# Optimization experiments

Hardware: AMD Instinct MI355X
Metric: run time of the kernel (lower is better)

The kernel has to match this reference:

```python
import jax, jax.numpy as jnp
import numpy as np

B, T, H = 4096, 64, 64        # sequences, time_step, n_hidden
OBS, ACT = 128, 32
EPS = 1e-12                    # tf.contrib layer_norm epsilon


def layer_norm(x, g, b):
    m = x.mean(-1, keepdims=True)
    v = x.var(-1, keepdims=True)
    return (x - m) * jax.lax.rsqrt(v + EPS) * g + b


def lstm_scan(xs, W, b):
    # xs: [T, B, D_in]; BasicLSTMCell with forget_bias=1.0
    h0 = jnp.zeros((xs.shape[1], H), xs.dtype)
    c0 = h0
    def step(carry, x_t):
        h, c = carry
        z = jnp.concatenate([x_t, h], axis=-1) @ W + b   # [B, 4H]
        i, j, f, o = jnp.split(z, 4, axis=-1)
        c = c * jax.nn.sigmoid(f + 1.0) + jax.nn.sigmoid(i) * jnp.tanh(j)
        h = jnp.tanh(c) * jax.nn.sigmoid(o)
        return (h, c), h
    _, hs = jax.lax.scan(step, (h0, c0), xs)
    return hs  # [T, B, H]


def setup_inputs() -> dict:
    key = jax.random.key(0)
    ks = jax.random.split(key, 10)
    u = lambda k, shp, s: jax.random.uniform(k, shp, jnp.float32, -s, s)
    return dict(
        obs=jax.random.normal(ks[0], (B * T, OBS), jnp.float32),
        action=jax.random.normal(ks[1], (B * T, ACT), jnp.float32),
        W1=u(ks[2], (OBS, 64), 0.1), b1=jnp.zeros(64), g1=jnp.ones(64), be1=jnp.zeros(64),
        W2=u(ks[3], (64 + ACT, 64), 0.1), b2=jnp.zeros(64), g2=jnp.ones(64), be2=jnp.zeros(64),
        Wf=u(ks[4], (64 + H, 4 * H), 0.08), bf=jnp.zeros(4 * H),
        Wb=u(ks[5], (64 + H, 4 * H), 0.08), bb=jnp.zeros(4 * H),
        wx=u(ks[6], (H,), 0.003), bx=jnp.zeros(()),
        wp=u(ks[7], (H,), 0.003), bp=jnp.zeros(()),
        gp=jnp.ones(T), bep=jnp.zeros(T),
        W3=u(ks[8], (T, T), 0.003), b3=jnp.zeros(T),
    )


def reference(obs, action, W1, b1, g1, be1, W2, b2, g2, be2,
              Wf, bf, Wb, bb, wx, bx, wp, bp, gp, bep, W3, b3):
    # MLP trunk
    x = jax.nn.relu(layer_norm(obs @ W1 + b1, g1, be1))
    x = jnp.concatenate([x, action], axis=-1)
    x = jax.nn.relu(layer_norm(x @ W2 + b2, g2, be2))
    # [B*T, 64] -> [T, B, 64] for scan
    x = x.reshape(B, T, 64).transpose(1, 0, 2)
    h_fw = lstm_scan(x, Wf, bf)                 # [T, B, H]
    h_bw = lstm_scan(x[::-1], Wb, bb)[::-1]     # [T, B, H]
    # tf.reshape of the (fw, bw) tuple stacks -> [2, B, T, H] -> [2B, T*H, 1]
    h = jnp.concatenate([h_fw.transpose(1, 0, 2), h_bw.transpose(1, 0, 2)], axis=0)  # [2B, T, H]
    # conv1d(kernel=H, stride=H) over flattened T*H axis == per-timestep dot
    xs = jnp.einsum('btd,d->bt', h, wx) + bx    # [2B, T] values
    ps = jnp.einsum('btd,d->bt', h, wp) + bp    # [2B, T] attention logits
    p = jax.nn.relu(layer_norm(ps, gp, bep))
    p = jax.nn.softmax(p @ W3 + b3, axis=-1)
    return jnp.sum(p * xs, axis=1)              # [2B]
```

## Files before the change

kernel.cpp:

```cpp
#include <hip/hip_runtime.h>
#include <hip/hip_bf16.h>

typedef __attribute__((ext_vector_type(8))) short s16x8;
typedef __attribute__((ext_vector_type(4))) float f32x4;

#define MFMA(a,b,c) __builtin_amdgcn_mfma_f32_16x16x32_bf16((a),(b),(c),0,0,0)

__device__ __forceinline__ unsigned short bf16_rne(float f){
  unsigned int u = __float_as_uint(f);
  return (unsigned short)((u + 0x7FFFu + ((u >> 16) & 1u)) >> 16);
}
__device__ __forceinline__ float bf16_f32(unsigned short h){
  return __uint_as_float(((unsigned int)h) << 16);
}
__device__ __forceinline__ void split_hl(float f, short& hi, short& lo){
  unsigned short h = bf16_rne(f);
  float rem = f - bf16_f32(h);
  hi = (short)h;
  lo = (short)bf16_rne(rem);
}

__device__ __forceinline__ void build_frag(const float* p, s16x8& fh, s16x8& fl){
  float4 v0 = *(const float4*)p;
  float4 v1 = *(const float4*)(p + 4);
  float vv[8] = {v0.x, v0.y, v0.z, v0.w, v1.x, v1.y, v1.z, v1.w};
  #pragma unroll
  for(int j = 0; j < 8; ++j){ short h, l; split_hl(vv[j], h, l); fh[j] = h; fl[j] = l; }
}

__device__ __forceinline__ float sigm(float x){
  return __builtin_amdgcn_rcpf(1.0f + __expf(-x));
}
__device__ __forceinline__ float tanh_fast(float x){
  return 1.0f - 2.0f * __builtin_amdgcn_rcpf(__expf(2.0f * x) + 1.0f);
}

__device__ __forceinline__ float red16(float x){
  int v;
  v = __builtin_amdgcn_update_dpp(0, __float_as_int(x), 0xB1, 0xF, 0xF, true);
  x += __int_as_float(v);
  v = __builtin_amdgcn_update_dpp(0, __float_as_int(x), 0x4E, 0xF, 0xF, true);
  x += __int_as_float(v);
  v = __builtin_amdgcn_update_dpp(0, __float_as_int(x), 0x141, 0xF, 0xF, true);
  x += __int_as_float(v);
  v = __builtin_amdgcn_update_dpp(0, __float_as_int(x), 0x140, 0xF, 0xF, true);
  x += __int_as_float(v);
  return x;
}

__global__ __launch_bounds__(256) void pack_kernel(
    const float* __restrict__ W1, const float* __restrict__ W2,
    const float* __restrict__ Wf, const float* __restrict__ Wb,
    unsigned short* __restrict__ w1p, unsigned short* __restrict__ w2p,
    unsigned short* __restrict__ wfp, unsigned short* __restrict__ wbp)
{
  int id = blockIdx.x * 256 + threadIdx.x;
  if(id < 8192){
    int t = id;
    int j = t & 7, lane = (t >> 3) & 63, nt = (t >> 9) & 3, kk = t >> 11;
    int k = kk * 32 + 8 * (lane >> 4) + j;
    int col = nt * 16 + (lane & 15);
    short h, l; split_hl(W1[k * 64 + col], h, l);
    w1p[t] = (unsigned short)h; w1p[8192 + t] = (unsigned short)l;
  } else if(id < 14336){
    int t = id - 8192;
    int j = t & 7, lane = (t >> 3) & 63, nt = (t >> 9) & 3, kk = t >> 11;
    int k = kk * 32 + 8 * (lane >> 4) + j;
    int col = nt * 16 + (lane & 15);
    short h, l; split_hl(W2[k * 64 + col], h, l);
    w2p[t] = (unsigned short)h; w2p[6144 + t] = (unsigned short)l;
  } else if(id < 47104){
    int t = id - 14336;
    int j = t & 7, lane = (t >> 3) & 63, dj = (t >> 9) & 3, kk = (t >> 11) & 3, gi = t >> 13;
    int k = kk * 32 + 8 * (lane >> 4) + j;
    int col = gi * 64 + dj * 16 + (lane & 15);
    short h, l; split_hl(Wf[k * 256 + col], h, l);
    wfp[t] = (unsigned short)h; wfp[32768 + t] = (unsigned short)l;
  } else if(id < 79872){
    int t = id - 47104;
    int j = t & 7, lane = (t >> 3) & 63, dj = (t >> 9) & 3, kk = (t >> 11) & 3, gi = t >> 13;
    int k = kk * 32 + 8 * (lane >> 4) + j;
    int col = gi * 64 + dj * 16 + (lane & 15);
    short h, l; split_hl(Wb[k * 256 + col], h, l);
    wbp[t] = (unsigned short)h; wbp[32768 + t] = (unsigned short)l;
  }
}

__global__ __launch_bounds__(256) void trunk_kernel(
    const float* __restrict__ obs, const float* __restrict__ actg,
    const float* __restrict__ b1, const float* __restrict__ g1, const float* __restrict__ be1,
    const float* __restrict__ b2, const float* __restrict__ g2, const float* __restrict__ be2,
    const unsigned short* __restrict__ w1p, const unsigned short* __restrict__ w2p,
    unsigned short* __restrict__ x2h, unsigned short* __restrict__ x2l)
{
  __shared__ __align__(16) float x1_t[64][68];

  const int tid = threadIdx.x;
  const int r0 = blockIdx.x * 64;
  const int w = tid >> 6, lane = tid & 63;
  const int l15 = lane & 15, l4 = lane >> 4;

  float b1v[4], g1v[4], be1v[4], b2v[4], g2v[4], be2v[4];
  #pragma unroll
  for(int nt = 0; nt < 4; ++nt){
    int col = nt * 16 + l15;
    b1v[nt] = b1[col]; g1v[nt] = g1[col]; be1v[nt] = be1[col];
    b2v[nt] = b2[col]; g2v[nt] = g2[col]; be2v[nt] = be2[col];
  }

  f32x4 acc1[4] = {{0,0,0,0},{0,0,0,0},{0,0,0,0},{0,0,0,0}};
  #pragma unroll
  for(int kk = 0; kk < 4; ++kk){
    s16x8 ah, al;
    build_frag(&obs[(size_t)(r0 + w * 16 + l15) * 128 + 8 * l4 + 32 * kk], ah, al);
    #pragma unroll
    for(int nt = 0; nt < 4; ++nt){
      s16x8 bh = *(const s16x8*)&w1p[(kk * 2048 + nt * 512) + lane * 8];
      s16x8 bl = *(const s16x8*)&w1p[8192 + (kk * 2048 + nt * 512) + lane * 8];
      acc1[nt] = MFMA(ah, bh, acc1[nt]);
      acc1[nt] = MFMA(ah, bl, acc1[nt]);
      acc1[nt] = MFMA(al, bh, acc1[nt]);
    }
  }

  #pragma unroll
  for(int r = 0; r < 4; ++r){
    float v[4];
    #pragma unroll
    for(int nt = 0; nt < 4; ++nt) v[nt] = acc1[nt][r] + b1v[nt];
    float s = (v[0] + v[1]) + (v[2] + v[3]);
    #pragma unroll
    for(int mm = 1; mm < 16; mm <<= 1) s += __shfl_xor(s, mm);
    float mean = s * (1.0f / 64.0f);
    float d[4]; float q = 0.f;
    #pragma unroll
    for(int nt = 0; nt < 4; ++nt){ d[nt] = v[nt] - mean; q += d[nt] * d[nt]; }
    #pragma unroll
    for(int mm = 1; mm < 16; mm <<= 1) q += __shfl_xor(q, mm);
    float rstd = rsqrtf(q * (1.0f / 64.0f) + 1e-12f);
    int row = w * 16 + l4 * 4 + r;
    #pragma unroll
    for(int nt = 0; nt < 4; ++nt)
      x1_t[row][nt * 16 + l15] = fmaxf(0.f, d[nt] * rstd * g1v[nt] + be1v[nt]);
  }
  __syncthreads();

  f32x4 acc2[4] = {{0,0,0,0},{0,0,0,0},{0,0,0,0},{0,0,0,0}};
  #pragma unroll
  for(int kk = 0; kk < 3; ++kk){
    s16x8 ah, al;
    if(kk < 2) build_frag(&x1_t[w * 16 + l15][8 * l4 + 32 * kk], ah, al);
    else       build_frag(&actg[(size_t)(r0 + w * 16 + l15) * 32 + 8 * l4], ah, al);
    #pragma unroll
    for(int nt = 0; nt < 4; ++nt){
      s16x8 bh = *(const s16x8*)&w2p[(kk * 2048 + nt * 512) + lane * 8];
      s16x8 bl = *(const s16x8*)&w2p[6144 + (kk * 2048 + nt * 512) + lane * 8];
      acc2[nt] = MFMA(ah, bh, acc2[nt]);
      acc2[nt] = MFMA(ah, bl, acc2[nt]);
      acc2[nt] = MFMA(al, bh, acc2[nt]);
    }
  }

  #pragma unroll
  for(int r = 0; r < 4; ++r){
    float v[4];
    #pragma unroll
    for(int nt = 0; nt < 4; ++nt) v[nt] = acc2[nt][r] + b2v[nt];
    float s = (v[0] + v[1]) + (v[2] + v[3]);
    #pragma unroll
    for(int mm = 1; mm < 16; mm <<= 1) s += __shfl_xor(s, mm);
    float mean = s * (1.0f / 64.0f);
    float d[4]; float q = 0.f;
    #pragma unroll
    for(int nt = 0; nt < 4; ++nt){ d[nt] = v[nt] - mean; q += d[nt] * d[nt]; }
    #pragma unroll
    for(int mm = 1; mm < 16; mm <<= 1) q += __shfl_xor(q, mm);
    float rstd = rsqrtf(q * (1.0f / 64.0f) + 1e-12f);
    size_t rowg = (size_t)(r0 + w * 16 + l4 * 4 + r);
    #pragma unroll
    for(int nt = 0; nt < 4; ++nt){
      float xv = fmaxf(0.f, d[nt] * rstd * g2v[nt] + be2v[nt]);
      short hi, lo; split_hl(xv, hi, lo);
      x2h[rowg * 64 + nt * 16 + l15] = (unsigned short)hi;
      x2l[rowg * 64 + nt * 16 + l15] = (unsigned short)lo;
    }
  }
}

__global__ __launch_bounds__(256, 2) void lstm_kernel(
    const unsigned short* __restrict__ x2h, const unsigned short* __restrict__ x2l,
    const unsigned short* __restrict__ wfp, const unsigned short* __restrict__ wbp,
    const float* __restrict__ bfv, const float* __restrict__ bbv,
    const float* __restrict__ wx, const float* __restrict__ wp,
    const float* __restrict__ bx, const float* __restrict__ bp,
    const float* __restrict__ gp, const float* __restrict__ bep,
    const float* __restrict__ W3, const float* __restrict__ b3,
    float* __restrict__ out)
{
  __shared__ __align__(16) unsigned short h_h[2][16][72];
  __shared__ __align__(16) unsigned short h_l[2][16][72];
  __shared__ float xs_part[2][4][16];
  __shared__ float ps_part[2][4][16];
  __shared__ float xs_sh[16][64];
  __shared__ float ps_sh[16][64];
  __shared__ float W3s[64][64];
  __shared__ float p_sh[4][64];

  const int tid = threadIdx.x;
  const int dir = blockIdx.y;
  const int b0 = blockIdx.x * 16;
  const unsigned short* wpk  = dir ? wbp : wfp;
  const float* bias = dir ? bbv : bfv;

  const int w = tid >> 6, lane = tid & 63, l15 = lane & 15, l4 = lane >> 4;
  const int dj = w;

  float biasv[4];
  #pragma unroll
  for(int gi = 0; gi < 4; ++gi) biasv[gi] = bias[gi * 64 + dj * 16 + l15];
  biasv[2] += 1.0f;
  const float wxv = wx[dj * 16 + l15];
  const float wpv = wp[dj * 16 + l15];

  s16x8 Bh[4][4], Bl[4][4];
  #pragma unroll
  for(int gi = 0; gi < 4; ++gi){
    #pragma unroll
    for(int kk = 0; kk < 4; ++kk){
      int off = ((gi * 4 + kk) * 4 + dj) * 512 + lane * 8;
      Bh[gi][kk] = *(const s16x8*)&wpk[off];
      Bl[gi][kk] = *(const s16x8*)&wpk[32768 + off];
    }
  }

  #pragma unroll
  for(int i = 0; i < 4; ++i)
    *(float4*)&W3s[0][tid * 16 + i * 4] = *(const float4*)&W3[tid * 16 + i * 4];
  for(int i = tid; i < 16 * 72; i += 256){
    (&h_h[0][0][0])[i] = 0; (&h_l[0][0][0])[i] = 0;
  }

  const unsigned short* xbh = x2h + (size_t)(b0 + l15) * 4096 + 8 * l4;
  const unsigned short* xbl = x2l + (size_t)(b0 + l15) * 4096 + 8 * l4;

  int t0 = dir ? 63 : 0;
  int t1 = dir ? 62 : 1;
  s16x8 xah  = *(const s16x8*)&xbh[t0 * 64];
  s16x8 xah2 = *(const s16x8*)&xbh[t0 * 64 + 32];
  s16x8 xal  = *(const s16x8*)&xbl[t0 * 64];
  s16x8 xal2 = *(const s16x8*)&xbl[t0 * 64 + 32];
  s16x8 xbhr = *(const s16x8*)&xbh[t1 * 64];
  s16x8 xbh2 = *(const s16x8*)&xbh[t1 * 64 + 32];
  s16x8 xblr = *(const s16x8*)&xbl[t1 * 64];
  s16x8 xbl2 = *(const s16x8*)&xbl[t1 * 64 + 32];

  float c[4] = {0.f, 0.f, 0.f, 0.f};

  __syncthreads();

  auto lstm_step = [&](s16x8& XH0, s16x8& XH1, s16x8& XL0, s16x8& XL1, int tau){
    const int cb = tau & 1, nb = cb ^ 1;
    if(tau > 0 && tid < 16){
      int pb = nb;
      int tp = dir ? 64 - tau : tau - 1;
      xs_sh[tid][tp] = (xs_part[pb][0][tid] + xs_part[pb][1][tid])
                     + (xs_part[pb][2][tid] + xs_part[pb][3][tid]);
      ps_sh[tid][tp] = (ps_part[pb][0][tid] + ps_part[pb][1][tid])
                     + (ps_part[pb][2][tid] + ps_part[pb][3][tid]);
    }
    s16x8 Ahh0 = *(const s16x8*)&h_h[cb][l15][8 * l4];
    s16x8 Ahh1 = *(const s16x8*)&h_h[cb][l15][8 * l4 + 32];
    s16x8 Ahl0 = *(const s16x8*)&h_l[cb][l15][8 * l4];
    s16x8 Ahl1 = *(const s16x8*)&h_l[cb][l15][8 * l4 + 32];
    f32x4 acc[4];
    #pragma unroll
    for(int gi = 0; gi < 4; ++gi)
      acc[gi] = (f32x4){biasv[gi], biasv[gi], biasv[gi], biasv[gi]};
    #pragma unroll
    for(int gi = 0; gi < 4; ++gi){
      acc[gi] = MFMA(XH0, Bh[gi][0], acc[gi]);
      acc[gi] = MFMA(XH0, Bl[gi][0], acc[gi]);
      acc[gi] = MFMA(XL0, Bh[gi][0], acc[gi]);
      acc[gi] = MFMA(XH1, Bh[gi][1], acc[gi]);
      acc[gi] = MFMA(XH1, Bl[gi][1], acc[gi]);
      acc[gi] = MFMA(XL1, Bh[gi][1], acc[gi]);
    }
    {
      int tf = tau + 2; if(tf > 63) tf = 63;
      int tn = dir ? 63 - tf : tf;
      XH0 = *(const s16x8*)&xbh[tn * 64];
      XH1 = *(const s16x8*)&xbh[tn * 64 + 32];
      XL0 = *(const s16x8*)&xbl[tn * 64];
      XL1 = *(const s16x8*)&xbl[tn * 64 + 32];
    }
    #pragma unroll
    for(int gi = 0; gi < 4; ++gi){
      acc[gi] = MFMA(Ahh0, Bh[gi][2], acc[gi]);
      acc[gi] = MFMA(Ahh0, Bl[gi][2], acc[gi]);
      acc[gi] = MFMA(Ahl0, Bh[gi][2], acc[gi]);
      acc[gi] = MFMA(Ahh1, Bh[gi][3], acc[gi]);
      acc[gi] = MFMA(Ahh1, Bl[gi][3], acc[gi]);
      acc[gi] = MFMA(Ahl1, Bh[gi][3], acc[gi]);
    }
    float hv[4];
    #pragma unroll
    for(int r = 0; r < 4; ++r){
      float zi = acc[0][r];
      float zj = acc[1][r];
      float zf = acc[2][r];
      float zo = acc[3][r];
      float cf = c[r] * sigm(zf) + sigm(zi) * tanh_fast(zj);
      c[r] = cf;
      hv[r] = tanh_fast(cf) * sigm(zo);
    }
    #pragma unroll
    for(int r = 0; r < 4; ++r){
      int s = l4 * 4 + r;
      short hi, lo; split_hl(hv[r], hi, lo);
      h_h[nb][s][dj * 16 + l15] = (unsigned short)hi;
      h_l[nb][s][dj * 16 + l15] = (unsigned short)lo;
    }
    #pragma unroll
    for(int r = 0; r < 4; ++r){
      float px = red16(hv[r] * wxv);
      float pp = red16(hv[r] * wpv);
      if(l15 == 0){
        int s = l4 * 4 + r;
        xs_part[cb][dj][s] = px;
        ps_part[cb][dj][s] = pp;
      }
    }
    __syncthreads();
  };

  for(int tau = 0; tau < 64; tau += 2){
    lstm_step(xah, xah2, xal, xal2, tau);
    lstm_step(xbhr, xbh2, xblr, xbl2, tau + 1);
  }

  if(tid < 16){
    int tp = dir ? 0 : 63;
    xs_sh[tid][tp] = (xs_part[1][0][tid] + xs_part[1][1][tid])
                   + (xs_part[1][2][tid] + xs_part[1][3][tid]);
    ps_sh[tid][tp] = (ps_part[1][0][tid] + ps_part[1][1][tid])
                   + (ps_part[1][2][tid] + ps_part[1][3][tid]);
  }
  __syncthreads();

  const float bxv = bx[0], bpv = bp[0];
  #pragma unroll
  for(int r = 0; r < 4; ++r){
    int s = w * 4 + r;
    float xsv = xs_sh[s][lane] + bxv;
    float psv = ps_sh[s][lane] + bpv;
    float sum = psv;
    #pragma unroll
    for(int mm = 1; mm < 64; mm <<= 1) sum += __shfl_xor(sum, mm);
    float mean = sum * (1.f / 64.f);
    float d = psv - mean;
    float q = d * d;
    #pragma unroll
    for(int mm = 1; mm < 64; mm <<= 1) q += __shfl_xor(q, mm);
    float rstd = rsqrtf(q * (1.f / 64.f) + 1e-12f);
    float p = fmaxf(0.f, d * rstd * gp[lane] + bep[lane]);
    p_sh[w][lane] = p;
    float logit = b3[lane];
    #pragma unroll 8
    for(int t = 0; t < 64; ++t) logit += p_sh[w][t] * W3s[t][lane];
    float mx = logit;
    #pragma unroll
    for(int mm = 1; mm < 64; mm <<= 1) mx = fmaxf(mx, __shfl_xor(mx, mm));
    float e = __expf(logit - mx);
    float se = e;
    #pragma unroll
    for(int mm = 1; mm < 64; mm <<= 1) se += __shfl_xor(se, mm);
    float contrib = (e / se) * xsv;
    #pragma unroll
    for(int mm = 1; mm < 64; mm <<= 1) contrib += __shfl_xor(contrib, mm);
    if(lane == 0) out[(size_t)dir * 4096 + b0 + s] = contrib;
  }
}

extern "C" void kernel_launch(void* const* d_in, const int* in_sizes, int n_in,
                              void* d_out, int out_size, void* d_ws, size_t ws_size,
                              hipStream_t stream)
{
  (void)in_sizes; (void)n_in; (void)out_size; (void)ws_size;
  const float* obs = (const float*)d_in[0];
  const float* act = (const float*)d_in[1];
  const float* W1  = (const float*)d_in[2];
  const float* b1  = (const float*)d_in[3];
  const float* g1  = (const float*)d_in[4];
  const float* be1 = (const float*)d_in[5];
  const float* W2  = (const float*)d_in[6];
  const float* b2  = (const float*)d_in[7];
  const float* g2  = (const float*)d_in[8];
  const float* be2 = (const float*)d_in[9];
  const float* Wf  = (const float*)d_in[10];
  const float* bfv = (const float*)d_in[11];
  const float* Wb  = (const float*)d_in[12];
  const float* bbv = (const float*)d_in[13];
  const float* wx  = (const float*)d_in[14];
  const float* bx  = (const float*)d_in[15];
  const float* wp  = (const float*)d_in[16];
  const float* bp  = (const float*)d_in[17];
  const float* gp  = (const float*)d_in[18];
  const float* bep = (const float*)d_in[19];
  const float* W3  = (const float*)d_in[20];
  const float* b3  = (const float*)d_in[21];

  unsigned short* x2h = (unsigned short*)d_ws;
  unsigned short* x2l = x2h + (size_t)262144 * 64;
  unsigned short* w1p = x2l + (size_t)262144 * 64;
  unsigned short* w2p = w1p + 2 * 8192;
  unsigned short* wfp = w2p + 2 * 6144;
  unsigned short* wbp = wfp + 2 * 32768;
  float* outf = (float*)d_out;

  pack_kernel<<<312, 256, 0, stream>>>(W1, W2, Wf, Wb, w1p, w2p, wfp, wbp);
  trunk_kernel<<<4096, 256, 0, stream>>>(obs, act, b1, g1, be1, b2, g2, be2, w1p, w2p, x2h, x2l);
  lstm_kernel<<<dim3(256, 2), 256, 0, stream>>>(x2h, x2l, wfp, wbp, bfv, bbv, wx, wp,
                                                bx, bp, gp, bep, W3, b3, outf);
}
```

Measured before the change: 176.7 us.

## Compute attention projections via MFMA on stored h and pack bf16 conversions

Replaces the per-step DPP reductions of h·wx and h·wp, and the cross-wave partial sums in shared memory, with four extra MFMAs issued by wave 0. These use the previous step's h fragments and a packed B operand holding the hi/lo splits of wx and wp. It also swaps scalar bf16 hi/lo splitting for the packed v_cvt_pk_bf16_f32 instruction, adds s_setprio around the MFMA blocks, and pins the weight registers with empty asm. The aim is fewer VALU and cross-lane operations in the serial recurrence, at the cost of uneven work on wave 0 and extra registers for Bx.

```diff
diff --git a/kernel.cpp b/kernel.cpp
--- a/kernel.cpp
+++ b/kernel.cpp
@@ -3,6 +3,7 @@
 
 typedef __attribute__((ext_vector_type(8))) short s16x8;
 typedef __attribute__((ext_vector_type(4))) float f32x4;
+typedef __attribute__((ext_vector_type(4))) unsigned int u32x4;
 
 #define MFMA(a,b,c) __builtin_amdgcn_mfma_f32_16x16x32_bf16((a),(b),(c),0,0,0)
 
@@ -20,12 +21,27 @@
   lo = (short)bf16_rne(rem);
 }
 
+__device__ __forceinline__ unsigned int cvt_pk_bf16(float a, float b){
+  unsigned int r;
+  asm("v_cvt_pk_bf16_f32 %0, %1, %2" : "=v"(r) : "v"(a), "v"(b));
+  return r;
+}
+
 __device__ __forceinline__ void build_frag(const float* p, s16x8& fh, s16x8& fl){
   float4 v0 = *(const float4*)p;
   float4 v1 = *(const float4*)(p + 4);
   float vv[8] = {v0.x, v0.y, v0.z, v0.w, v1.x, v1.y, v1.z, v1.w};
-  #pragma unroll
-  for(int j = 0; j < 8; ++j){ short h, l; split_hl(vv[j], h, l); fh[j] = h; fl[j] = l; }
+  u32x4 th, tl;
+  #pragma unroll
+  for(int q = 0; q < 4; ++q){
+    unsigned int h2 = cvt_pk_bf16(vv[2*q], vv[2*q+1]);
+    float r0 = vv[2*q]     - __uint_as_float(h2 << 16);
+    float r1 = vv[2*q + 1] - __uint_as_float(h2 & 0xffff0000u);
+    th[q] = h2;
+    tl[q] = cvt_pk_bf16(r0, r1);
+  }
+  fh = __builtin_bit_cast(s16x8, th);
+  fl = __builtin_bit_cast(s16x8, tl);
 }
 
 __device__ __forceinline__ float sigm(float x){
@@ -33,19 +49,6 @@
 }
 __device__ __forceinline__ float tanh_fast(float x){
   return 1.0f - 2.0f * __builtin_amdgcn_rcpf(__expf(2.0f * x) + 1.0f);
-}
-
-__device__ __forceinline__ float red16(float x){
-  int v;
-  v = __builtin_amdgcn_update_dpp(0, __float_as_int(x), 0xB1, 0xF, 0xF, true);
-  x += __int_as_float(v);
-  v = __builtin_amdgcn_update_dpp(0, __float_as_int(x), 0x4E, 0xF, 0xF, true);
-  x += __int_as_float(v);
-  v = __builtin_amdgcn_update_dpp(0, __float_as_int(x), 0x141, 0xF, 0xF, true);
-  x += __int_as_float(v);
-  v = __builtin_amdgcn_update_dpp(0, __float_as_int(x), 0x140, 0xF, 0xF, true);
-  x += __int_as_float(v);
-  return x;
 }
 
 __global__ __launch_bounds__(256) void pack_kernel(
@@ -177,13 +180,25 @@
     for(int mm = 1; mm < 16; mm <<= 1) q += __shfl_xor(q, mm);
     float rstd = rsqrtf(q * (1.0f / 64.0f) + 1e-12f);
     size_t rowg = (size_t)(r0 + w * 16 + l4 * 4 + r);
-    #pragma unroll
-    for(int nt = 0; nt < 4; ++nt){
-      float xv = fmaxf(0.f, d[nt] * rstd * g2v[nt] + be2v[nt]);
-      short hi, lo; split_hl(xv, hi, lo);
-      x2h[rowg * 64 + nt * 16 + l15] = (unsigned short)hi;
-      x2l[rowg * 64 + nt * 16 + l15] = (unsigned short)lo;
-    }
+    float xv[4];
+    #pragma unroll
+    for(int nt = 0; nt < 4; ++nt) xv[nt] = fmaxf(0.f, d[nt] * rstd * g2v[nt] + be2v[nt]);
+    unsigned int ph01 = cvt_pk_bf16(xv[0], xv[1]);
+    float q0 = xv[0] - __uint_as_float(ph01 << 16);
+    float q1 = xv[1] - __uint_as_float(ph01 & 0xffff0000u);
+    unsigned int pl01 = cvt_pk_bf16(q0, q1);
+    unsigned int ph23 = cvt_pk_bf16(xv[2], xv[3]);
+    float q2 = xv[2] - __uint_as_float(ph23 << 16);
+    float q3 = xv[3] - __uint_as_float(ph23 & 0xffff0000u);
+    unsigned int pl23 = cvt_pk_bf16(q2, q3);
+    x2h[rowg * 64 +  0 + l15] = (unsigned short)ph01;
+    x2h[rowg * 64 + 16 + l15] = (unsigned short)(ph01 >> 16);
+    x2h[rowg * 64 + 32 + l15] = (unsigned short)ph23;
+    x2h[rowg * 64 + 48 + l15] = (unsigned short)(ph23 >> 16);
+    x2l[rowg * 64 +  0 + l15] = (unsigned short)pl01;
+    x2l[rowg * 64 + 16 + l15] = (unsigned short)(pl01 >> 16);
+    x2l[rowg * 64 + 32 + l15] = (unsigned short)pl23;
+    x2l[rowg * 64 + 48 + l15] = (unsigned short)(pl23 >> 16);
   }
 }
 
@@ -199,8 +214,6 @@
 {
   __shared__ __align__(16) unsigned short h_h[2][16][72];
   __shared__ __align__(16) unsigned short h_l[2][16][72];
-  __shared__ float xs_part[2][4][16];
-  __shared__ float ps_part[2][4][16];
   __shared__ float xs_sh[16][64];
   __shared__ float ps_sh[16][64];
   __shared__ float W3s[64][64];
@@ -219,8 +232,6 @@
   #pragma unroll
   for(int gi = 0; gi < 4; ++gi) biasv[gi] = bias[gi * 64 + dj * 16 + l15];
   biasv[2] += 1.0f;
-  const float wxv = wx[dj * 16 + l15];
-  const float wpv = wp[dj * 16 + l15];
 
   s16x8 Bh[4][4], Bl[4][4];
   #pragma unroll
@@ -230,6 +241,21 @@
       int off = ((gi * 4 + kk) * 4 + dj) * 512 + lane * 8;
       Bh[gi][kk] = *(const s16x8*)&wpk[off];
       Bl[gi][kk] = *(const s16x8*)&wpk[32768 + off];
+      asm volatile("" : "+v"(Bh[gi][kk]), "+v"(Bl[gi][kk]));
+    }
+  }
+
+  s16x8 Bx[2];
+  #pragma unroll
+  for(int kk = 0; kk < 2; ++kk){
+    #pragma unroll
+    for(int j = 0; j < 8; ++j){
+      int k = kk * 32 + 8 * l4 + j;
+      short xh, xl, ph, pl;
+      split_hl(wx[k], xh, xl);
+      split_hl(wp[k], ph, pl);
+      short sel = (l15 == 0) ? xh : (l15 == 1) ? xl : (l15 == 2) ? ph : (l15 == 3) ? pl : (short)0;
+      Bx[kk][j] = sel;
     }
   }
 
@@ -260,14 +286,6 @@
 
   auto lstm_step = [&](s16x8& XH0, s16x8& XH1, s16x8& XL0, s16x8& XL1, int tau){
     const int cb = tau & 1, nb = cb ^ 1;
-    if(tau > 0 && tid < 16){
-      int pb = nb;
-      int tp = dir ? 64 - tau : tau - 1;
-      xs_sh[tid][tp] = (xs_part[pb][0][tid] + xs_part[pb][1][tid])
-                     + (xs_part[pb][2][tid] + xs_part[pb][3][tid]);
-      ps_sh[tid][tp] = (ps_part[pb][0][tid] + ps_part[pb][1][tid])
-                     + (ps_part[pb][2][tid] + ps_part[pb][3][tid]);
-    }
     s16x8 Ahh0 = *(const s16x8*)&h_h[cb][l15][8 * l4];
     s16x8 Ahh1 = *(const s16x8*)&h_h[cb][l15][8 * l4 + 32];
     s16x8 Ahl0 = *(const s16x8*)&h_l[cb][l15][8 * l4];
@@ -276,6 +294,7 @@
     #pragma unroll
     for(int gi = 0; gi < 4; ++gi)
       acc[gi] = (f32x4){biasv[gi], biasv[gi], biasv[gi], biasv[gi]};
+    __builtin_amdgcn_s_setprio(1);
     #pragma unroll
     for(int gi = 0; gi < 4; ++gi){
       acc[gi] = MFMA(XH0, Bh[gi][0], acc[gi]);
@@ -285,6 +304,7 @@
       acc[gi] = MFMA(XH1, Bl[gi][1], acc[gi]);
       acc[gi] = MFMA(XL1, Bh[gi][1], acc[gi]);
     }
+    __builtin_amdgcn_s_setprio(0);
     {
       int tf = tau + 2; if(tf > 63) tf = 63;
       int tn = dir ? 63 - tf : tf;
@@ -293,6 +313,8 @@
       XL0 = *(const s16x8*)&xbl[tn * 64];
       XL1 = *(const s16x8*)&xbl[tn * 64 + 32];
     }
+    f32x4 accd = {0.f, 0.f, 0.f, 0.f};
+    __builtin_amdgcn_s_setprio(1);
     #pragma unroll
     for(int gi = 0; gi < 4; ++gi){
       acc[gi] = MFMA(Ahh0, Bh[gi][2], acc[gi]);
@@ -301,6 +323,23 @@
       acc[gi] = MFMA(Ahh1, Bh[gi][3], acc[gi]);
       acc[gi] = MFMA(Ahh1, Bl[gi][3], acc[gi]);
       acc[gi] = MFMA(Ahl1, Bh[gi][3], acc[gi]);
+    }
+    if(dj == 0){
+      accd = MFMA(Ahh0, Bx[0], accd);
+      accd = MFMA(Ahl0, Bx[0], accd);
+      accd = MFMA(Ahh1, Bx[1], accd);
+      accd = MFMA(Ahl1, Bx[1], accd);
+    }
+    __builtin_amdgcn_s_setprio(0);
+    if(dj == 0 && tau > 0){
+      int tp = dir ? 64 - tau : tau - 1;
+      #pragma unroll
+      for(int r = 0; r < 4; ++r){
+        float v = accd[r] + __shfl_xor(accd[r], 1);
+        int s = l4 * 4 + r;
+        if(l15 == 0) xs_sh[s][tp] = v;
+        else if(l15 == 2) ps_sh[s][tp] = v;
+      }
     }
     float hv[4];
     #pragma unroll
@@ -313,22 +352,24 @@
       c[r] = cf;
       hv[r] = tanh_fast(cf) * sigm(zo);
     }
-    #pragma unroll
-    for(int r = 0; r < 4; ++r){
-      int s = l4 * 4 + r;
-      short hi, lo; split_hl(hv[r], hi, lo);
-      h_h[nb][s][dj * 16 + l15] = (unsigned short)hi;
-      h_l[nb][s][dj * 16 + l15] = (unsigned short)lo;
-    }
-    #pragma unroll
-    for(int r = 0; r < 4; ++r){
-      float px = red16(hv[r] * wxv);
-      float pp = red16(hv[r] * wpv);
-      if(l15 == 0){
-        int s = l4 * 4 + r;
-        xs_part[cb][dj][s] = px;
-        ps_part[cb][dj][s] = pp;
-      }
+    {
+      unsigned int ph01 = cvt_pk_bf16(hv[0], hv[1]);
+      float q0 = hv[0] - __uint_as_float(ph01 << 16);
+      float q1 = hv[1] - __uint_as_float(ph01 & 0xffff0000u);
+      unsigned int pl01 = cvt_pk_bf16(q0, q1);
+      unsigned int ph23 = cvt_pk_bf16(hv[2], hv[3]);
+      float q2 = hv[2] - __uint_as_float(ph23 << 16);
+      float q3 = hv[3] - __uint_as_float(ph23 & 0xffff0000u);
+      unsigned int pl23 = cvt_pk_bf16(q2, q3);
+      int sb = l4 * 4, col = dj * 16 + l15;
+      h_h[nb][sb + 0][col] = (unsigned short)ph01;
+      h_h[nb][sb + 1][col] = (unsigned short)(ph01 >> 16);
+      h_h[nb][sb + 2][col] = (unsigned short)ph23;
+      h_h[nb][sb + 3][col] = (unsigned short)(ph23 >> 16);
+      h_l[nb][sb + 0][col] = (unsigned short)pl01;
+      h_l[nb][sb + 1][col] = (unsigned short)(pl01 >> 16);
+      h_l[nb][sb + 2][col] = (unsigned short)pl23;
+      h_l[nb][sb + 3][col] = (unsigned short)(pl23 >> 16);
     }
     __syncthreads();
   };
@@ -338,12 +379,24 @@
     lstm_step(xbhr, xbh2, xblr, xbl2, tau + 1);
   }
 
-  if(tid < 16){
+  if(dj == 0){
+    s16x8 Ahh0 = *(const s16x8*)&h_h[0][l15][8 * l4];
+    s16x8 Ahh1 = *(const s16x8*)&h_h[0][l15][8 * l4 + 32];
+    s16x8 Ahl0 = *(const s16x8*)&h_l[0][l15][8 * l4];
+    s16x8 Ahl1 = *(const s16x8*)&h_l[0][l15][8 * l4 + 32];
+    f32x4 accd = {0.f, 0.f, 0.f, 0.f};
+    accd = MFMA(Ahh0, Bx[0], accd);
+    accd = MFMA(Ahl0, Bx[0], accd);
+    accd = MFMA(Ahh1, Bx[1], accd);
+    accd = MFMA(Ahl1, Bx[1], accd);
     int tp = dir ? 0 : 63;
-    xs_sh[tid][tp] = (xs_part[1][0][tid] + xs_part[1][1][tid])
-                   + (xs_part[1][2][tid] + xs_part[1][3][tid]);
-    ps_sh[tid][tp] = (ps_part[1][0][tid] + ps_part[1][1][tid])
-                   + (ps_part[1][2][tid] + ps_part[1][3][tid]);
+    #pragma unroll
+    for(int r = 0; r < 4; ++r){
+      float v = accd[r] + __shfl_xor(accd[r], 1);
+      int s = l4 * 4 + r;
+      if(l15 == 0) xs_sh[s][tp] = v;
+      else if(l15 == 2) ps_sh[s][tp] = v;
+    }
   }
   __syncthreads();
 
```

After: 183.0 us. +3.5%, slower.
